# Kernel optimization log

Hardware: AMD Instinct MI355X
Metric: run time of the kernel (lower is better)

## Reference

```python
import jax, jax.numpy as jnp
import numpy as np
import math

B, P, N = 4, 8, 512
D_MODEL, H, D_K = 128, 4, 32
T_ALL = 4
WHICH_IDX = np.array([0, 1, 3])  # which_transition_matrices = [T,T,F,T]
T = 3
EPS = 1e-5


def setup_inputs() -> dict:
    key = jax.random.key(0)
    ks = jax.random.split(key, 12)
    inputs = jax.random.normal(ks[0], (B, P, N, D_MODEL), jnp.float32)
    c_inputs = jax.random.normal(ks[1], (B, P, N, D_MODEL), jnp.float32)
    vals = jax.random.uniform(ks[2], (T_ALL, N, N), jnp.float32)
    keep = (jax.random.uniform(ks[3], (T_ALL, N, N)) < 0.05).astype(jnp.float32)
    eye = jnp.eye(N, dtype=jnp.float32)
    transition_matrices = vals * keep * (1.0 - eye) + eye
    s = 1.0 / math.sqrt(D_MODEL)
    Wq = jax.random.normal(ks[4], (T, D_MODEL, D_MODEL), jnp.float32) * s
    Wk = jax.random.normal(ks[5], (T, D_MODEL, D_MODEL), jnp.float32) * s
    Wv = jax.random.normal(ks[6], (T, D_MODEL, D_MODEL), jnp.float32) * s
    Wo = jax.random.normal(ks[7], (D_MODEL, T * D_MODEL), jnp.float32) * (1.0 / math.sqrt(T * D_MODEL))
    ln_gamma = jnp.ones((D_MODEL,), jnp.float32)
    ln_beta = jnp.zeros((D_MODEL,), jnp.float32)
    return dict(inputs=inputs, c_inputs=c_inputs, transition_matrices=transition_matrices,
                Wq=Wq, Wk=Wk, Wv=Wv, Wo=Wo, ln_gamma=ln_gamma, ln_beta=ln_beta)


def reference(inputs, c_inputs, transition_matrices, Wq, Wk, Wv, Wo, ln_gamma, ln_beta):
    tm = transition_matrices[jnp.asarray(WHICH_IDX)]  # [T, N, N]
    # per-transition-matrix projections (torch Linear: x @ W.T), then split heads
    def proj(W):
        y = jnp.einsum('bpnd,tod->tbpno', inputs, W)
        return y.reshape(T, B, P, N, H, D_K)
    Q, K, V = proj(Wq), proj(Wk), proj(Wv)
    scores = jnp.einsum('tbpnhk,tbpmhk->tbphnm', Q, K) / math.sqrt(D_K)
    mask = jnp.where(tm != 0, 0.0, -jnp.inf)[:, None, None, None]  # [T,1,1,1,N,N]
    alpha = jax.nn.softmax(scores + mask, axis=-1)
    # post-softmax reweighting by transition matrix, then V matmul
    out = jnp.einsum('tbphnm,tbpmhk->tbpnhk', alpha * tm[:, None, None, None], V)
    out = out.reshape(T, B, P, N, D_MODEL)
    out = jnp.moveaxis(out, 0, -2).reshape(B, P, N, T * D_MODEL)  # concat over matrices
    out = jnp.einsum('bpnf,df->bpnd', out, Wo)  # final Linear (bias=False); dropout p=0
    res = out + inputs
    mu = res.mean(-1, keepdims=True)
    var = ((res - mu) ** 2).mean(-1, keepdims=True)
    return (res - mu) / jnp.sqrt(var + EPS) * ln_gamma + ln_beta
```

## Files before the change

### kernel.cpp

```cpp
#include <hip/hip_runtime.h>


typedef __attribute__((ext_vector_type(8))) short  short8;
typedef __attribute__((ext_vector_type(4))) float  floatx4;

#define WS_BIG   50331648ull
#define WS_XL    54919168ull
#define QSCALE   0.25503486f

__device__ __forceinline__ float b2f(unsigned short u) {
    union { unsigned int i; float f; } v; v.i = ((unsigned int)u) << 16; return v.f;
}
__device__ __forceinline__ unsigned short f2b(float f) {
    union { float f; unsigned int i; } v; v.f = f;
    unsigned int x = v.i;
    return (unsigned short)((x + 0x7fffu + ((x >> 16) & 1u)) >> 16);
}
__device__ __forceinline__ short8 cvt8(const float* p) {
    floatx4 a = *(const floatx4*)p;
    floatx4 b = *(const floatx4*)(p + 4);
    short8 r;
    r[0] = (short)f2b(a[0]); r[1] = (short)f2b(a[1]);
    r[2] = (short)f2b(a[2]); r[3] = (short)f2b(a[3]);
    r[4] = (short)f2b(b[0]); r[5] = (short)f2b(b[1]);
    r[6] = (short)f2b(b[2]); r[7] = (short)f2b(b[3]);
    return r;
}

__global__ __launch_bounds__(256) void k_prep(
    const float* __restrict__ X,  const float* __restrict__ Wq,
    const float* __restrict__ Wk, const float* __restrict__ Wv,
    const float* __restrict__ Wo,
    unsigned short* __restrict__ Xb, unsigned short* __restrict__ Wb,
    unsigned short* __restrict__ Wob)
{
    size_t i = ((size_t)blockIdx.x * 256 + threadIdx.x) * 8;
    const float* src; unsigned short* dst; size_t off;
    if      (i < 2097152) { src = X;  dst = Xb;          off = i; }
    else if (i < 2146304) { src = Wq; dst = Wb;          off = i - 2097152; }
    else if (i < 2195456) { src = Wk; dst = Wb + 49152;  off = i - 2146304; }
    else if (i < 2244608) { src = Wv; dst = Wb + 98304;  off = i - 2195456; }
    else                  { src = Wo; dst = Wob;         off = i - 2244608; }
    *(short8*)&dst[off] = cvt8(&src[off]);
}

__global__ __launch_bounds__(256) void k_qkv_pre(
    const unsigned short* __restrict__ Xb,
    const unsigned short* __restrict__ Wb,
    unsigned short* __restrict__ q_ws,
    unsigned short* __restrict__ k_ws,
    unsigned short* __restrict__ v_ws)
{
    int bp = blockIdx.x, mt = blockIdx.y, tz = blockIdx.z;
    __shared__ unsigned short Xs[128 * 128];
    int tid = threadIdx.x;
    int lane = tid & 63, wv = tid >> 6;
    int l15 = lane & 15, quad = lane >> 4;

    const unsigned short* Xbase = Xb + ((size_t)bp * 512 + mt * 128) * 128;
    for (int i = 0; i < 8; ++i) {
        int e = (i * 256 + tid) * 8;
        *(short8*)&Xs[e] = *(const short8*)&Xbase[e];
    }
    __syncthreads();

    unsigned short* Osel[3] = { q_ws, k_ws, v_ws };
    for (int qkv = 0; qkv < 3; ++qkv) {
        const unsigned short* Wt = Wb + qkv * 49152 + tz * 16384;
        unsigned short* Ob = Osel[qkv] + (size_t)tz * 2097152
                           + ((size_t)bp * 512 + mt * 128) * 128;
        float sc = (qkv == 0) ? QSCALE : 1.0f;
        for (int ct = 0; ct < 8; ++ct) {
            short8 bfr[4];
            for (int kk = 0; kk < 4; ++kk)
                bfr[kk] = *(const short8*)&Wt[(size_t)(ct * 16 + l15) * 128 + kk * 32 + quad * 8];
            floatx4 acc0 = {0.f, 0.f, 0.f, 0.f};
            floatx4 acc1 = {0.f, 0.f, 0.f, 0.f};
            int rt0 = wv * 2, rt1 = wv * 2 + 1;
            for (int kk = 0; kk < 4; ++kk) {
                short8 a0 = *(const short8*)&Xs[(rt0 * 16 + l15) * 128 + kk * 32 + quad * 8];
                short8 a1 = *(const short8*)&Xs[(rt1 * 16 + l15) * 128 + kk * 32 + quad * 8];
                acc0 = __builtin_amdgcn_mfma_f32_16x16x32_bf16(a0, bfr[kk], acc0, 0, 0, 0);
                acc1 = __builtin_amdgcn_mfma_f32_16x16x32_bf16(a1, bfr[kk], acc1, 0, 0, 0);
            }
            int col = ct * 16 + l15;
            for (int i = 0; i < 4; ++i) {
                Ob[(size_t)(rt0 * 16 + quad * 4 + i) * 128 + col] = f2b(acc0[i] * sc);
                Ob[(size_t)(rt1 * 16 + quad * 4 + i) * 128 + col] = f2b(acc1[i] * sc);
            }
        }
    }
}

__global__ __launch_bounds__(256) void k_qkv_cvt(
    const float* __restrict__ X,
    const float* __restrict__ Wq, const float* __restrict__ Wk,
    const float* __restrict__ Wv,
    unsigned short* __restrict__ q_ws, unsigned short* __restrict__ k_ws,
    unsigned short* __restrict__ v_ws,
    int wstride, int ostride)
{
    int bp = blockIdx.x, mt = blockIdx.y, tz = blockIdx.z;
    __shared__ unsigned short Xs[128 * 128];
    int tid = threadIdx.x;
    int lane = tid & 63, wv = tid >> 6;
    int l15 = lane & 15, quad = lane >> 4;

    const float* Xbase = X + ((size_t)bp * 512 + mt * 128) * 128;
    for (int i = 0; i < 8; ++i) {
        int e = (i * 256 + tid) * 8;
        *(short8*)&Xs[e] = cvt8(&Xbase[e]);
    }
    __syncthreads();

    size_t woff = (size_t)tz * wstride;
    size_t ooff = (size_t)tz * ostride;
    const float* Wsel[3] = { Wq + woff, Wk + woff, Wv + woff };
    unsigned short* Osel[3] = { q_ws + ooff, k_ws + ooff, v_ws + ooff };

    for (int qkv = 0; qkv < 3; ++qkv) {
        const float* Wb = Wsel[qkv];
        unsigned short* Ob = Osel[qkv] + ((size_t)bp * 512 + mt * 128) * 128;
        float sc = (qkv == 0) ? QSCALE : 1.0f;
        for (int ct = 0; ct < 8; ++ct) {
            short8 bfr[4];
            for (int kk = 0; kk < 4; ++kk)
                bfr[kk] = cvt8(&Wb[(size_t)(ct * 16 + l15) * 128 + kk * 32 + quad * 8]);
            floatx4 acc0 = {0.f, 0.f, 0.f, 0.f};
            floatx4 acc1 = {0.f, 0.f, 0.f, 0.f};
            int rt0 = wv * 2, rt1 = wv * 2 + 1;
            for (int kk = 0; kk < 4; ++kk) {
                short8 a0 = *(const short8*)&Xs[(rt0 * 16 + l15) * 128 + kk * 32 + quad * 8];
                short8 a1 = *(const short8*)&Xs[(rt1 * 16 + l15) * 128 + kk * 32 + quad * 8];
                acc0 = __builtin_amdgcn_mfma_f32_16x16x32_bf16(a0, bfr[kk], acc0, 0, 0, 0);
                acc1 = __builtin_amdgcn_mfma_f32_16x16x32_bf16(a1, bfr[kk], acc1, 0, 0, 0);
            }
            int col = ct * 16 + l15;
            for (int i = 0; i < 4; ++i) {
                Ob[(size_t)(rt0 * 16 + quad * 4 + i) * 128 + col] = f2b(acc0[i] * sc);
                Ob[(size_t)(rt1 * 16 + quad * 4 + i) * 128 + col] = f2b(acc1[i] * sc);
            }
        }
    }
}

__global__ __launch_bounds__(512) void k_attn(
    const unsigned short* __restrict__ q_ws,
    const unsigned short* __restrict__ k_ws,
    const unsigned short* __restrict__ v_ws,
    const float* __restrict__ tm,
    unsigned short* __restrict__ att_ws,
    int qkv_stride, int toff0)
{
    int nc = blockIdx.x;
    int bp = blockIdx.y;
    int z  = blockIdx.z;
    int t = z >> 2, h = z & 3;
    size_t qoff = (size_t)t * (size_t)qkv_stride;
    const float* tmt = tm + (size_t)(t + (t >> 1)) * 262144;
    int toff = toff0 + t * 128;

    __shared__ unsigned short Vt[32][516];
    __shared__ unsigned short Ps[8][16][72];

    int tid = threadIdx.x, lane = tid & 63, wv = tid >> 6;
    int l15 = lane & 15, quad = lane >> 4;

    {
        const unsigned short* vp = v_ws + qoff + ((size_t)bp * 512 + tid) * 128 + h * 32;
        short8 a = *(const short8*)vp;
        short8 b = *(const short8*)(vp + 8);
        short8 c = *(const short8*)(vp + 16);
        short8 d = *(const short8*)(vp + 24);
        #pragma unroll
        for (int j = 0; j < 8; ++j) {
            Vt[j][tid]      = (unsigned short)a[j];
            Vt[8 + j][tid]  = (unsigned short)b[j];
            Vt[16 + j][tid] = (unsigned short)c[j];
            Vt[24 + j][tid] = (unsigned short)d[j];
        }
    }
    int n0 = nc * 128 + wv * 16;
    short8 qf = *(const short8*)&q_ws[qoff +
        ((size_t)bp * 512 + n0 + l15) * 128 + h * 32 + quad * 8];
    __syncthreads();

    const unsigned short* Kb = k_ws + qoff + (size_t)bp * 512 * 128 + h * 32;
    floatx4 O0 = {0.f, 0.f, 0.f, 0.f};
    floatx4 O1 = {0.f, 0.f, 0.f, 0.f};
    float za[4] = {0.f, 0.f, 0.f, 0.f};
    const floatx4 zero4 = {0.f, 0.f, 0.f, 0.f};

    for (int c = 0; c < 8; ++c) {
        int mb = c * 64;
        short8 kf0 = *(const short8*)&Kb[(size_t)(mb +  0 + l15) * 128 + quad * 8];
        short8 kf1 = *(const short8*)&Kb[(size_t)(mb + 16 + l15) * 128 + quad * 8];
        short8 kf2 = *(const short8*)&Kb[(size_t)(mb + 32 + l15) * 128 + quad * 8];
        short8 kf3 = *(const short8*)&Kb[(size_t)(mb + 48 + l15) * 128 + quad * 8];
        floatx4 S[4];
        S[0] = __builtin_amdgcn_mfma_f32_16x16x32_bf16(qf, kf0, zero4, 0, 0, 0);
        S[1] = __builtin_amdgcn_mfma_f32_16x16x32_bf16(qf, kf1, zero4, 0, 0, 0);
        S[2] = __builtin_amdgcn_mfma_f32_16x16x32_bf16(qf, kf2, zero4, 0, 0, 0);
        S[3] = __builtin_amdgcn_mfma_f32_16x16x32_bf16(qf, kf3, zero4, 0, 0, 0);

        #pragma unroll
        for (int ti = 0; ti < 4; ++ti) {
            int m = mb + ti * 16 + l15;
            #pragma unroll
            for (int i = 0; i < 4; ++i) {
                float tmv = tmt[(size_t)(n0 + quad * 4 + i) * 512 + m];
                float e = __builtin_amdgcn_exp2f(S[ti][i]);
                bool on = (tmv != 0.0f);
                za[i] += on ? e : 0.0f;
                float w = on ? e * tmv : 0.0f;
                Ps[wv][quad * 4 + i][ti * 16 + l15] = f2b(w);
            }
        }
        #pragma unroll
        for (int kc = 0; kc < 2; ++kc) {
            short8 pa  = *(const short8*)&Ps[wv][l15][kc * 32 + quad * 8];
            short8 vb0 = *(const short8*)&Vt[l15][mb + kc * 32 + quad * 8];
            short8 vb1 = *(const short8*)&Vt[16 + l15][mb + kc * 32 + quad * 8];
            O0 = __builtin_amdgcn_mfma_f32_16x16x32_bf16(pa, vb0, O0, 0, 0, 0);
            O1 = __builtin_amdgcn_mfma_f32_16x16x32_bf16(pa, vb1, O1, 0, 0, 0);
        }
    }

    #pragma unroll
    for (int d = 1; d < 16; d <<= 1) {
        #pragma unroll
        for (int i = 0; i < 4; ++i) za[i] += __shfl_xor(za[i], d, 64);
    }
    #pragma unroll
    for (int i = 0; i < 4; ++i) {
        float rz = 1.0f / za[i];
        size_t row = (size_t)bp * 512 + n0 + quad * 4 + i;
        att_ws[row * 384 + toff + h * 32 + l15]      = f2b(O0[i] * rz);
        att_ws[row * 384 + toff + h * 32 + 16 + l15] = f2b(O1[i] * rz);
    }
}

__global__ __launch_bounds__(256) void k_oproj_pre(
    const unsigned short* __restrict__ att_ws,
    const unsigned short* __restrict__ Wob,
    const float* __restrict__ X,
    const float* __restrict__ gamma,
    const float* __restrict__ beta,
    float* __restrict__ out)
{
    int bp = blockIdx.x;
    int mt = blockIdx.y;
    __shared__ unsigned short As[64 * 128];
    __shared__ unsigned short Ws[128 * 128];
    int tid = threadIdx.x, lane = tid & 63, wv = tid >> 6;
    int l15 = lane & 15, quad = lane >> 4;

    floatx4 acc[8];
    for (int ct = 0; ct < 8; ++ct) acc[ct] = (floatx4){0.f, 0.f, 0.f, 0.f};
    size_t rowbase = (size_t)bp * 512 + mt * 64;

    for (int kc = 0; kc < 3; ++kc) {
        __syncthreads();
        for (int i = 0; i < 4; ++i) {
            int flat = i * 256 + tid;
            int row = flat >> 4, colg = (flat & 15) * 8;
            *(short8*)&As[row * 128 + colg] =
                *(const short8*)&att_ws[(rowbase + row) * 384 + kc * 128 + colg];
        }
        for (int i = 0; i < 8; ++i) {
            int flat = i * 256 + tid;
            int row = flat >> 4, colg = (flat & 15) * 8;
            *(short8*)&Ws[row * 128 + colg] =
                *(const short8*)&Wob[(size_t)row * 384 + kc * 128 + colg];
        }
        __syncthreads();
        for (int ct = 0; ct < 8; ++ct) {
            for (int kk = 0; kk < 4; ++kk) {
                short8 a = *(const short8*)&As[(wv * 16 + l15) * 128 + kk * 32 + quad * 8];
                short8 b = *(const short8*)&Ws[(ct * 16 + l15) * 128 + kk * 32 + quad * 8];
                acc[ct] = __builtin_amdgcn_mfma_f32_16x16x32_bf16(a, b, acc[ct], 0, 0, 0);
            }
        }
    }

    for (int i = 0; i < 4; ++i) {
        int lrow = wv * 16 + quad * 4 + i;
        size_t grow = rowbase + lrow;
        float vals[8];
        float s = 0.f, sq = 0.f;
        for (int ct = 0; ct < 8; ++ct) {
            int col = ct * 16 + l15;
            float v = acc[ct][i] + X[grow * 128 + col];
            vals[ct] = v;
            s += v; sq += v * v;
        }
        for (int d = 1; d < 16; d <<= 1) {
            s  += __shfl_xor(s, d, 64);
            sq += __shfl_xor(sq, d, 64);
        }
        float mu = s * (1.0f / 128.0f);
        float var = sq * (1.0f / 128.0f) - mu * mu;
        float rs = rsqrtf(var + 1e-5f);
        for (int ct = 0; ct < 8; ++ct) {
            int col = ct * 16 + l15;
            out[grow * 128 + col] = (vals[ct] - mu) * rs * gamma[col] + beta[col];
        }
    }
}

__global__ __launch_bounds__(256) void k_oproj_cvt(
    const unsigned short* __restrict__ att_ws,
    const float* __restrict__ Wo,
    const float* __restrict__ X,
    const float* __restrict__ gamma,
    const float* __restrict__ beta,
    float* __restrict__ out)
{
    int bp = blockIdx.x;
    int mt = blockIdx.y;
    __shared__ unsigned short As[64 * 128];
    __shared__ unsigned short Ws[128 * 128];
    int tid = threadIdx.x, lane = tid & 63, wv = tid >> 6;
    int l15 = lane & 15, quad = lane >> 4;

    floatx4 acc[8];
    for (int ct = 0; ct < 8; ++ct) acc[ct] = (floatx4){0.f, 0.f, 0.f, 0.f};
    size_t rowbase = (size_t)bp * 512 + mt * 64;

    for (int kc = 0; kc < 3; ++kc) {
        __syncthreads();
        for (int i = 0; i < 4; ++i) {
            int flat = i * 256 + tid;
            int row = flat >> 4, colg = (flat & 15) * 8;
            *(short8*)&As[row * 128 + colg] =
                *(const short8*)&att_ws[(rowbase + row) * 384 + kc * 128 + colg];
        }
        for (int i = 0; i < 8; ++i) {
            int flat = i * 256 + tid;
            int row = flat >> 4, colg = (flat & 15) * 8;
            *(short8*)&Ws[row * 128 + colg] = cvt8(&Wo[(size_t)row * 384 + kc * 128 + colg]);
        }
        __syncthreads();
        for (int ct = 0; ct < 8; ++ct) {
            for (int kk = 0; kk < 4; ++kk) {
                short8 a = *(const short8*)&As[(wv * 16 + l15) * 128 + kk * 32 + quad * 8];
                short8 b = *(const short8*)&Ws[(ct * 16 + l15) * 128 + kk * 32 + quad * 8];
                acc[ct] = __builtin_amdgcn_mfma_f32_16x16x32_bf16(a, b, acc[ct], 0, 0, 0);
            }
        }
    }

    for (int i = 0; i < 4; ++i) {
        int lrow = wv * 16 + quad * 4 + i;
        size_t grow = rowbase + lrow;
        float vals[8];
        float s = 0.f, sq = 0.f;
        for (int ct = 0; ct < 8; ++ct) {
            int col = ct * 16 + l15;
            float v = acc[ct][i] + X[grow * 128 + col];
            vals[ct] = v;
            s += v; sq += v * v;
        }
        for (int d = 1; d < 16; d <<= 1) {
            s  += __shfl_xor(s, d, 64);
            sq += __shfl_xor(sq, d, 64);
        }
        float mu = s * (1.0f / 128.0f);
        float var = sq * (1.0f / 128.0f) - mu * mu;
        float rs = rsqrtf(var + 1e-5f);
        for (int ct = 0; ct < 8; ++ct) {
            int col = ct * 16 + l15;
            out[grow * 128 + col] = (vals[ct] - mu) * rs * gamma[col] + beta[col];
        }
    }
}

extern "C" void kernel_launch(void* const* d_in, const int* in_sizes, int n_in,
                              void* d_out, int out_size, void* d_ws, size_t ws_size,
                              hipStream_t stream) {
    const float* X     = (const float*)d_in[0];
    const float* TM    = (const float*)d_in[2];
    const float* Wq    = (const float*)d_in[3];
    const float* Wk    = (const float*)d_in[4];
    const float* Wv    = (const float*)d_in[5];
    const float* Wo    = (const float*)d_in[6];
    const float* gamma = (const float*)d_in[7];
    const float* beta  = (const float*)d_in[8];
    float* out = (float*)d_out;

    char* ws = (char*)d_ws;
    const size_t QKV1 = 2097152;
    const size_t QKV1B = QKV1 * 2;

    if (ws_size >= WS_XL) {
        unsigned short* q3  = (unsigned short*)(ws);
        unsigned short* k3  = (unsigned short*)(ws + 3 * QKV1B);
        unsigned short* v3  = (unsigned short*)(ws + 6 * QKV1B);
        unsigned short* att = (unsigned short*)(ws + 9 * QKV1B);
        unsigned short* Xb  = (unsigned short*)(ws + 50331648ull);
        unsigned short* Wb  = (unsigned short*)(ws + 54525952ull);
        unsigned short* Wob = (unsigned short*)(ws + 54820864ull);
        k_prep<<<dim3(1120), 256, 0, stream>>>(X, Wq, Wk, Wv, Wo, Xb, Wb, Wob);
        k_qkv_pre<<<dim3(32, 4, 3), 256, 0, stream>>>(Xb, Wb, q3, k3, v3);
        k_attn<<<dim3(4, 32, 12), 512, 0, stream>>>(q3, k3, v3, TM, att, (int)QKV1, 0);
        k_oproj_pre<<<dim3(32, 8), 256, 0, stream>>>(att, Wob, X, gamma, beta, out);
    } else if (ws_size >= WS_BIG) {
        unsigned short* q3  = (unsigned short*)(ws);
        unsigned short* k3  = (unsigned short*)(ws + 3 * QKV1B);
        unsigned short* v3  = (unsigned short*)(ws + 6 * QKV1B);
        unsigned short* att = (unsigned short*)(ws + 9 * QKV1B);
        k_qkv_cvt<<<dim3(32, 4, 3), 256, 0, stream>>>(
            X, Wq, Wk, Wv, q3, k3, v3, 16384, (int)QKV1);
        k_attn<<<dim3(4, 32, 12), 512, 0, stream>>>(q3, k3, v3, TM, att, (int)QKV1, 0);
        k_oproj_cvt<<<dim3(32, 8), 256, 0, stream>>>(att, Wo, X, gamma, beta, out);
    } else {
        unsigned short* q_ws   = (unsigned short*)(ws);
        unsigned short* k_ws   = (unsigned short*)(ws + QKV1B);
        unsigned short* v_ws   = (unsigned short*)(ws + 2 * QKV1B);
        unsigned short* att_ws = (unsigned short*)(ws + 3 * QKV1B);
        const int tsel[3] = {0, 1, 3};
        for (int t = 0; t < 3; ++t) {
            k_qkv_cvt<<<dim3(32, 4, 1), 256, 0, stream>>>(
                X, Wq + (size_t)t * 16384, Wk + (size_t)t * 16384, Wv + (size_t)t * 16384,
                q_ws, k_ws, v_ws, 0, 0);
            k_attn<<<dim3(4, 32, 4), 512, 0, stream>>>(
                q_ws, k_ws, v_ws, TM + (size_t)tsel[t] * 262144, att_ws, 0, t * 128);
        }
        k_oproj_cvt<<<dim3(32, 8), 256, 0, stream>>>(att_ws, Wo, X, gamma, beta, out);
    }
}
```

Baseline: 191.0 us.

## Pre-transpose transition matrices to bf16 and widen QKV/oproj grids

The prep kernel no longer converts X to bf16. Instead it transposes the three selected transition matrices into bf16 so the attention kernel can read a column-contiguous 4-element vector per lane instead of strided fp32 values. The QKV kernel now splits q/k/v across the grid z dimension (9 slices) and converts X inline. The output projection uses 32-row tiles with a cross-wave LayerNorm reduction through shared memory, which doubles its block count. The costs are redundant X conversion across the 9 z-slices and bf16 rounding of the transition weights.

```diff
diff --git a/kernel.cpp b/kernel.cpp
--- a/kernel.cpp
+++ b/kernel.cpp
@@ -3,9 +3,10 @@
 
 typedef __attribute__((ext_vector_type(8))) short  short8;
 typedef __attribute__((ext_vector_type(4))) float  floatx4;
+typedef __attribute__((ext_vector_type(4))) unsigned short u16x4;
 
 #define WS_BIG   50331648ull
-#define WS_XL    54919168ull
+#define WS_XL    52297728ull
 #define QSCALE   0.25503486f
 
 __device__ __forceinline__ float b2f(unsigned short u) {
@@ -15,6 +16,9 @@
     union { float f; unsigned int i; } v; v.f = f;
     unsigned int x = v.i;
     return (unsigned short)((x + 0x7fffu + ((x >> 16) & 1u)) >> 16);
+}
+__device__ __forceinline__ unsigned int fbits(float f) {
+    union { float f; unsigned int i; } v; v.f = f; return v.i;
 }
 __device__ __forceinline__ short8 cvt8(const float* p) {
     floatx4 a = *(const floatx4*)p;
@@ -28,28 +32,106 @@
 }
 
 __global__ __launch_bounds__(256) void k_prep(
-    const float* __restrict__ X,  const float* __restrict__ Wq,
-    const float* __restrict__ Wk, const float* __restrict__ Wv,
-    const float* __restrict__ Wo,
-    unsigned short* __restrict__ Xb, unsigned short* __restrict__ Wb,
-    unsigned short* __restrict__ Wob)
-{
-    size_t i = ((size_t)blockIdx.x * 256 + threadIdx.x) * 8;
-    const float* src; unsigned short* dst; size_t off;
-    if      (i < 2097152) { src = X;  dst = Xb;          off = i; }
-    else if (i < 2146304) { src = Wq; dst = Wb;          off = i - 2097152; }
-    else if (i < 2195456) { src = Wk; dst = Wb + 49152;  off = i - 2146304; }
-    else if (i < 2244608) { src = Wv; dst = Wb + 98304;  off = i - 2195456; }
-    else                  { src = Wo; dst = Wob;         off = i - 2244608; }
-    *(short8*)&dst[off] = cvt8(&src[off]);
-}
-
-__global__ __launch_bounds__(256) void k_qkv_pre(
-    const unsigned short* __restrict__ Xb,
+    const float* __restrict__ Wq, const float* __restrict__ Wk,
+    const float* __restrict__ Wv, const float* __restrict__ Wo,
+    const float* __restrict__ TM,
+    unsigned short* __restrict__ Wb,
+    unsigned short* __restrict__ Wob,
+    unsigned short* __restrict__ tmT)
+{
+    int bid = blockIdx.x, tid = threadIdx.x;
+    if (bid < 96) {
+        size_t i = (size_t)bid * 2048 + tid * 8;
+        const float* src; unsigned short* dst; size_t off;
+        if      (i <  49152) { src = Wq; dst = Wb;          off = i; }
+        else if (i <  98304) { src = Wk; dst = Wb + 49152;  off = i - 49152; }
+        else if (i < 147456) { src = Wv; dst = Wb + 98304;  off = i - 98304; }
+        else                 { src = Wo; dst = Wob;         off = i - 147456; }
+        *(short8*)&dst[off] = cvt8(&src[off]);
+        return;
+    }
+    __shared__ float Tl[64][65];
+    int r = bid - 96;
+    int t = r >> 6, tile = r & 63;
+    int ntile = tile >> 3, mtile = tile & 7;
+    const float* tmsrc = TM + (size_t)(t + (t >> 1)) * 262144;
+    {
+        int row = tid >> 2, cseg = (tid & 3) * 16;
+        const float* p = &tmsrc[(size_t)(ntile * 64 + row) * 512 + mtile * 64 + cseg];
+        #pragma unroll
+        for (int j = 0; j < 4; ++j)
+            *(floatx4*)&Tl[row][cseg + j * 4] = *(const floatx4*)&p[j * 4];
+    }
+    __syncthreads();
+    {
+        int m = tid >> 2, nseg = (tid & 3) * 16;
+        unsigned short* q = &tmT[(size_t)t * 262144 +
+                                 (size_t)(mtile * 64 + m) * 512 + ntile * 64 + nseg];
+        short8 o0, o1;
+        #pragma unroll
+        for (int j = 0; j < 8; ++j) {
+            o0[j] = (short)f2b(Tl[nseg + j][m]);
+            o1[j] = (short)f2b(Tl[nseg + 8 + j][m]);
+        }
+        *(short8*)&q[0] = o0;
+        *(short8*)&q[8] = o1;
+    }
+}
+
+__global__ __launch_bounds__(256) void k_qkv2(
+    const float* __restrict__ X,
     const unsigned short* __restrict__ Wb,
     unsigned short* __restrict__ q_ws,
     unsigned short* __restrict__ k_ws,
     unsigned short* __restrict__ v_ws)
+{
+    int bp = blockIdx.x, mt = blockIdx.y, z = blockIdx.z;
+    int t = z / 3, qkv = z - t * 3;
+    __shared__ unsigned short Xs[128 * 128];
+    int tid = threadIdx.x;
+    int lane = tid & 63, wv = tid >> 6;
+    int l15 = lane & 15, quad = lane >> 4;
+
+    const float* Xbase = X + ((size_t)bp * 512 + mt * 128) * 128;
+    for (int i = 0; i < 8; ++i) {
+        int e = (i * 256 + tid) * 8;
+        *(short8*)&Xs[e] = cvt8(&Xbase[e]);
+    }
+    __syncthreads();
+
+    const unsigned short* Wt = Wb + qkv * 49152 + t * 16384;
+    unsigned short* Ob = (qkv == 0 ? q_ws : qkv == 1 ? k_ws : v_ws)
+                       + (size_t)t * 2097152 + ((size_t)bp * 512 + mt * 128) * 128;
+    float sc = (qkv == 0) ? QSCALE : 1.0f;
+
+    for (int ct = 0; ct < 8; ++ct) {
+        short8 bfr[4];
+        for (int kk = 0; kk < 4; ++kk)
+            bfr[kk] = *(const short8*)&Wt[(size_t)(ct * 16 + l15) * 128 + kk * 32 + quad * 8];
+        floatx4 acc0 = {0.f, 0.f, 0.f, 0.f};
+        floatx4 acc1 = {0.f, 0.f, 0.f, 0.f};
+        int rt0 = wv * 2, rt1 = wv * 2 + 1;
+        for (int kk = 0; kk < 4; ++kk) {
+            short8 a0 = *(const short8*)&Xs[(rt0 * 16 + l15) * 128 + kk * 32 + quad * 8];
+            short8 a1 = *(const short8*)&Xs[(rt1 * 16 + l15) * 128 + kk * 32 + quad * 8];
+            acc0 = __builtin_amdgcn_mfma_f32_16x16x32_bf16(a0, bfr[kk], acc0, 0, 0, 0);
+            acc1 = __builtin_amdgcn_mfma_f32_16x16x32_bf16(a1, bfr[kk], acc1, 0, 0, 0);
+        }
+        int col = ct * 16 + l15;
+        for (int i = 0; i < 4; ++i) {
+            Ob[(size_t)(rt0 * 16 + quad * 4 + i) * 128 + col] = f2b(acc0[i] * sc);
+            Ob[(size_t)(rt1 * 16 + quad * 4 + i) * 128 + col] = f2b(acc1[i] * sc);
+        }
+    }
+}
+
+__global__ __launch_bounds__(256) void k_qkv_cvt(
+    const float* __restrict__ X,
+    const float* __restrict__ Wq, const float* __restrict__ Wk,
+    const float* __restrict__ Wv,
+    unsigned short* __restrict__ q_ws, unsigned short* __restrict__ k_ws,
+    unsigned short* __restrict__ v_ws,
+    int wstride, int ostride)
 {
     int bp = blockIdx.x, mt = blockIdx.y, tz = blockIdx.z;
     __shared__ unsigned short Xs[128 * 128];
@@ -57,23 +139,26 @@
     int lane = tid & 63, wv = tid >> 6;
     int l15 = lane & 15, quad = lane >> 4;
 
-    const unsigned short* Xbase = Xb + ((size_t)bp * 512 + mt * 128) * 128;
+    const float* Xbase = X + ((size_t)bp * 512 + mt * 128) * 128;
     for (int i = 0; i < 8; ++i) {
         int e = (i * 256 + tid) * 8;
-        *(short8*)&Xs[e] = *(const short8*)&Xbase[e];
+        *(short8*)&Xs[e] = cvt8(&Xbase[e]);
     }
     __syncthreads();
 
-    unsigned short* Osel[3] = { q_ws, k_ws, v_ws };
+    size_t woff = (size_t)tz * wstride;
+    size_t ooff = (size_t)tz * ostride;
+    const float* Wsel[3] = { Wq + woff, Wk + woff, Wv + woff };
+    unsigned short* Osel[3] = { q_ws + ooff, k_ws + ooff, v_ws + ooff };
+
     for (int qkv = 0; qkv < 3; ++qkv) {
-        const unsigned short* Wt = Wb + qkv * 49152 + tz * 16384;
-        unsigned short* Ob = Osel[qkv] + (size_t)tz * 2097152
-                           + ((size_t)bp * 512 + mt * 128) * 128;
+        const float* Wt = Wsel[qkv];
+        unsigned short* Ob = Osel[qkv] + ((size_t)bp * 512 + mt * 128) * 128;
         float sc = (qkv == 0) ? QSCALE : 1.0f;
         for (int ct = 0; ct < 8; ++ct) {
             short8 bfr[4];
             for (int kk = 0; kk < 4; ++kk)
-                bfr[kk] = *(const short8*)&Wt[(size_t)(ct * 16 + l15) * 128 + kk * 32 + quad * 8];
+                bfr[kk] = cvt8(&Wt[(size_t)(ct * 16 + l15) * 128 + kk * 32 + quad * 8]);
             floatx4 acc0 = {0.f, 0.f, 0.f, 0.f};
             floatx4 acc1 = {0.f, 0.f, 0.f, 0.f};
             int rt0 = wv * 2, rt1 = wv * 2 + 1;
@@ -92,59 +177,105 @@
     }
 }
 
-__global__ __launch_bounds__(256) void k_qkv_cvt(
-    const float* __restrict__ X,
-    const float* __restrict__ Wq, const float* __restrict__ Wk,
-    const float* __restrict__ Wv,
-    unsigned short* __restrict__ q_ws, unsigned short* __restrict__ k_ws,
-    unsigned short* __restrict__ v_ws,
-    int wstride, int ostride)
-{
-    int bp = blockIdx.x, mt = blockIdx.y, tz = blockIdx.z;
-    __shared__ unsigned short Xs[128 * 128];
-    int tid = threadIdx.x;
-    int lane = tid & 63, wv = tid >> 6;
+__global__ __launch_bounds__(512) void k_attn_t(
+    const unsigned short* __restrict__ q_ws,
+    const unsigned short* __restrict__ k_ws,
+    const unsigned short* __restrict__ v_ws,
+    const unsigned short* __restrict__ tmT,
+    unsigned short* __restrict__ att_ws)
+{
+    int nc = blockIdx.x;
+    int bp = blockIdx.y;
+    int z  = blockIdx.z;
+    int t = z >> 2, h = z & 3;
+    size_t qoff = (size_t)t * 2097152;
+    const unsigned short* tmt = tmT + (size_t)t * 262144;
+
+    __shared__ unsigned short Vt[32][516];
+    __shared__ unsigned short Ps[8][16][72];
+
+    int tid = threadIdx.x, lane = tid & 63, wv = tid >> 6;
     int l15 = lane & 15, quad = lane >> 4;
 
-    const float* Xbase = X + ((size_t)bp * 512 + mt * 128) * 128;
-    for (int i = 0; i < 8; ++i) {
-        int e = (i * 256 + tid) * 8;
-        *(short8*)&Xs[e] = cvt8(&Xbase[e]);
-    }
+    {
+        const unsigned short* vp = v_ws + qoff + ((size_t)bp * 512 + tid) * 128 + h * 32;
+        short8 a = *(const short8*)vp;
+        short8 b = *(const short8*)(vp + 8);
+        short8 c = *(const short8*)(vp + 16);
+        short8 d = *(const short8*)(vp + 24);
+        #pragma unroll
+        for (int j = 0; j < 8; ++j) {
+            Vt[j][tid]      = (unsigned short)a[j];
+            Vt[8 + j][tid]  = (unsigned short)b[j];
+            Vt[16 + j][tid] = (unsigned short)c[j];
+            Vt[24 + j][tid] = (unsigned short)d[j];
+        }
+    }
+    int n0 = nc * 128 + wv * 16;
+    short8 qf = *(const short8*)&q_ws[qoff +
+        ((size_t)bp * 512 + n0 + l15) * 128 + h * 32 + quad * 8];
     __syncthreads();
 
-    size_t woff = (size_t)tz * wstride;
-    size_t ooff = (size_t)tz * ostride;
-    const float* Wsel[3] = { Wq + woff, Wk + woff, Wv + woff };
-    unsigned short* Osel[3] = { q_ws + ooff, k_ws + ooff, v_ws + ooff };
-
-    for (int qkv = 0; qkv < 3; ++qkv) {
-        const float* Wb = Wsel[qkv];
-        unsigned short* Ob = Osel[qkv] + ((size_t)bp * 512 + mt * 128) * 128;
-        float sc = (qkv == 0) ? QSCALE : 1.0f;
-        for (int ct = 0; ct < 8; ++ct) {
-            short8 bfr[4];
-            for (int kk = 0; kk < 4; ++kk)
-                bfr[kk] = cvt8(&Wb[(size_t)(ct * 16 + l15) * 128 + kk * 32 + quad * 8]);
-            floatx4 acc0 = {0.f, 0.f, 0.f, 0.f};
-            floatx4 acc1 = {0.f, 0.f, 0.f, 0.f};
-            int rt0 = wv * 2, rt1 = wv * 2 + 1;
-            for (int kk = 0; kk < 4; ++kk) {
-                short8 a0 = *(const short8*)&Xs[(rt0 * 16 + l15) * 128 + kk * 32 + quad * 8];
-                short8 a1 = *(const short8*)&Xs[(rt1 * 16 + l15) * 128 + kk * 32 + quad * 8];
-                acc0 = __builtin_amdgcn_mfma_f32_16x16x32_bf16(a0, bfr[kk], acc0, 0, 0, 0);
-                acc1 = __builtin_amdgcn_mfma_f32_16x16x32_bf16(a1, bfr[kk], acc1, 0, 0, 0);
+    const unsigned short* Kb = k_ws + qoff + (size_t)bp * 512 * 128 + h * 32;
+    floatx4 O0 = {0.f, 0.f, 0.f, 0.f};
+    floatx4 O1 = {0.f, 0.f, 0.f, 0.f};
+    float za[4] = {0.f, 0.f, 0.f, 0.f};
+    const floatx4 zero4 = {0.f, 0.f, 0.f, 0.f};
+
+    for (int c = 0; c < 8; ++c) {
+        int mb = c * 64;
+        short8 kf0 = *(const short8*)&Kb[(size_t)(mb +  0 + l15) * 128 + quad * 8];
+        short8 kf1 = *(const short8*)&Kb[(size_t)(mb + 16 + l15) * 128 + quad * 8];
+        short8 kf2 = *(const short8*)&Kb[(size_t)(mb + 32 + l15) * 128 + quad * 8];
+        short8 kf3 = *(const short8*)&Kb[(size_t)(mb + 48 + l15) * 128 + quad * 8];
+        u16x4 t4[4];
+        #pragma unroll
+        for (int ti = 0; ti < 4; ++ti)
+            t4[ti] = *(const u16x4*)&tmt[(size_t)(mb + ti * 16 + l15) * 512 + n0 + quad * 4];
+        floatx4 S[4];
+        S[0] = __builtin_amdgcn_mfma_f32_16x16x32_bf16(qf, kf0, zero4, 0, 0, 0);
+        S[1] = __builtin_amdgcn_mfma_f32_16x16x32_bf16(qf, kf1, zero4, 0, 0, 0);
+        S[2] = __builtin_amdgcn_mfma_f32_16x16x32_bf16(qf, kf2, zero4, 0, 0, 0);
+        S[3] = __builtin_amdgcn_mfma_f32_16x16x32_bf16(qf, kf3, zero4, 0, 0, 0);
+
+        #pragma unroll
+        for (int ti = 0; ti < 4; ++ti) {
+            #pragma unroll
+            for (int i = 0; i < 4; ++i) {
+                unsigned short tv = t4[ti][i];
+                float e = __builtin_amdgcn_exp2f(S[ti][i]);
+                bool on = (tv != 0);
+                za[i] += on ? e : 0.0f;
+                float w = on ? e * b2f(tv) : 0.0f;
+                Ps[wv][quad * 4 + i][ti * 16 + l15] =
+                    (unsigned short)((fbits(w) + 0x8000u) >> 16);
             }
-            int col = ct * 16 + l15;
-            for (int i = 0; i < 4; ++i) {
-                Ob[(size_t)(rt0 * 16 + quad * 4 + i) * 128 + col] = f2b(acc0[i] * sc);
-                Ob[(size_t)(rt1 * 16 + quad * 4 + i) * 128 + col] = f2b(acc1[i] * sc);
-            }
-        }
-    }
-}
-
-__global__ __launch_bounds__(512) void k_attn(
+        }
+        #pragma unroll
+        for (int kc = 0; kc < 2; ++kc) {
+            short8 pa  = *(const short8*)&Ps[wv][l15][kc * 32 + quad * 8];
+            short8 vb0 = *(const short8*)&Vt[l15][mb + kc * 32 + quad * 8];
+            short8 vb1 = *(const short8*)&Vt[16 + l15][mb + kc * 32 + quad * 8];
+            O0 = __builtin_amdgcn_mfma_f32_16x16x32_bf16(pa, vb0, O0, 0, 0, 0);
+            O1 = __builtin_amdgcn_mfma_f32_16x16x32_bf16(pa, vb1, O1, 0, 0, 0);
+        }
+    }
+
+    #pragma unroll
+    for (int d = 1; d < 16; d <<= 1) {
+        #pragma unroll
+        for (int i = 0; i < 4; ++i) za[i] += __shfl_xor(za[i], d, 64);
+    }
+    #pragma unroll
+    for (int i = 0; i < 4; ++i) {
+        float rz = 1.0f / za[i];
+        size_t row = (size_t)bp * 512 + n0 + quad * 4 + i;
+        att_ws[row * 384 + t * 128 + h * 32 + l15]      = f2b(O0[i] * rz);
+        att_ws[row * 384 + t * 128 + h * 32 + 16 + l15] = f2b(O1[i] * rz);
+    }
+}
+
+__global__ __launch_bounds__(512) void k_attn_f32(
     const unsigned short* __restrict__ q_ws,
     const unsigned short* __restrict__ k_ws,
     const unsigned short* __restrict__ v_ws,
@@ -240,7 +371,7 @@
     }
 }
 
-__global__ __launch_bounds__(256) void k_oproj_pre(
+__global__ __launch_bounds__(256) void k_oproj2(
     const unsigned short* __restrict__ att_ws,
     const unsigned short* __restrict__ Wob,
     const float* __restrict__ X,
@@ -250,18 +381,20 @@
 {
     int bp = blockIdx.x;
     int mt = blockIdx.y;
-    __shared__ unsigned short As[64 * 128];
+    __shared__ unsigned short As[32 * 128];
     __shared__ unsigned short Ws[128 * 128];
+    __shared__ float psum[2][2][16][2];
     int tid = threadIdx.x, lane = tid & 63, wv = tid >> 6;
     int l15 = lane & 15, quad = lane >> 4;
-
-    floatx4 acc[8];
-    for (int ct = 0; ct < 8; ++ct) acc[ct] = (floatx4){0.f, 0.f, 0.f, 0.f};
-    size_t rowbase = (size_t)bp * 512 + mt * 64;
+    int rt = wv >> 1, ch = wv & 1;
+
+    floatx4 acc[4];
+    for (int c4 = 0; c4 < 4; ++c4) acc[c4] = (floatx4){0.f, 0.f, 0.f, 0.f};
+    size_t rowbase = (size_t)bp * 512 + mt * 32;
 
     for (int kc = 0; kc < 3; ++kc) {
         __syncthreads();
-        for (int i = 0; i < 4; ++i) {
+        for (int i = 0; i < 2; ++i) {
             int flat = i * 256 + tid;
             int row = flat >> 4, colg = (flat & 15) * 8;
             *(short8*)&As[row * 128 + colg] =
@@ -274,36 +407,47 @@
                 *(const short8*)&Wob[(size_t)row * 384 + kc * 128 + colg];
         }
         __syncthreads();
-        for (int ct = 0; ct < 8; ++ct) {
+        for (int c4 = 0; c4 < 4; ++c4) {
+            int ct = ch * 4 + c4;
             for (int kk = 0; kk < 4; ++kk) {
-                short8 a = *(const short8*)&As[(wv * 16 + l15) * 128 + kk * 32 + quad * 8];
+                short8 a = *(const short8*)&As[(rt * 16 + l15) * 128 + kk * 32 + quad * 8];
                 short8 b = *(const short8*)&Ws[(ct * 16 + l15) * 128 + kk * 32 + quad * 8];
-                acc[ct] = __builtin_amdgcn_mfma_f32_16x16x32_bf16(a, b, acc[ct], 0, 0, 0);
+                acc[c4] = __builtin_amdgcn_mfma_f32_16x16x32_bf16(a, b, acc[c4], 0, 0, 0);
             }
         }
     }
 
+    float vals[4][4], ssum[4], qsum[4];
     for (int i = 0; i < 4; ++i) {
-        int lrow = wv * 16 + quad * 4 + i;
-        size_t grow = rowbase + lrow;
-        float vals[8];
+        size_t grow = rowbase + rt * 16 + quad * 4 + i;
         float s = 0.f, sq = 0.f;
-        for (int ct = 0; ct < 8; ++ct) {
-            int col = ct * 16 + l15;
-            float v = acc[ct][i] + X[grow * 128 + col];
-            vals[ct] = v;
+        for (int c4 = 0; c4 < 4; ++c4) {
+            int col = (ch * 4 + c4) * 16 + l15;
+            float v = acc[c4][i] + X[grow * 128 + col];
+            vals[i][c4] = v;
             s += v; sq += v * v;
         }
         for (int d = 1; d < 16; d <<= 1) {
             s  += __shfl_xor(s, d, 64);
             sq += __shfl_xor(sq, d, 64);
         }
+        ssum[i] = s; qsum[i] = sq;
+        if (l15 == 0) {
+            psum[ch][rt][quad * 4 + i][0] = s;
+            psum[ch][rt][quad * 4 + i][1] = sq;
+        }
+    }
+    __syncthreads();
+    for (int i = 0; i < 4; ++i) {
+        size_t grow = rowbase + rt * 16 + quad * 4 + i;
+        float s  = ssum[i] + psum[ch ^ 1][rt][quad * 4 + i][0];
+        float sq = qsum[i] + psum[ch ^ 1][rt][quad * 4 + i][1];
         float mu = s * (1.0f / 128.0f);
         float var = sq * (1.0f / 128.0f) - mu * mu;
         float rs = rsqrtf(var + 1e-5f);
-        for (int ct = 0; ct < 8; ++ct) {
-            int col = ct * 16 + l15;
-            out[grow * 128 + col] = (vals[ct] - mu) * rs * gamma[col] + beta[col];
+        for (int c4 = 0; c4 < 4; ++c4) {
+            int col = (ch * 4 + c4) * 16 + l15;
+            out[grow * 128 + col] = (vals[i][c4] - mu) * rs * gamma[col] + beta[col];
         }
     }
 }
@@ -393,17 +537,17 @@
     const size_t QKV1B = QKV1 * 2;
 
     if (ws_size >= WS_XL) {
-        unsigned short* q3  = (unsigned short*)(ws);
-        unsigned short* k3  = (unsigned short*)(ws + 3 * QKV1B);
-        unsigned short* v3  = (unsigned short*)(ws + 6 * QKV1B);
-        unsigned short* att = (unsigned short*)(ws + 9 * QKV1B);
-        unsigned short* Xb  = (unsigned short*)(ws + 50331648ull);
-        unsigned short* Wb  = (unsigned short*)(ws + 54525952ull);
-        unsigned short* Wob = (unsigned short*)(ws + 54820864ull);
-        k_prep<<<dim3(1120), 256, 0, stream>>>(X, Wq, Wk, Wv, Wo, Xb, Wb, Wob);
-        k_qkv_pre<<<dim3(32, 4, 3), 256, 0, stream>>>(Xb, Wb, q3, k3, v3);
-        k_attn<<<dim3(4, 32, 12), 512, 0, stream>>>(q3, k3, v3, TM, att, (int)QKV1, 0);
-        k_oproj_pre<<<dim3(32, 8), 256, 0, stream>>>(att, Wob, X, gamma, beta, out);
+        unsigned short* q3   = (unsigned short*)(ws);
+        unsigned short* k3   = (unsigned short*)(ws + 3 * QKV1B);
+        unsigned short* v3   = (unsigned short*)(ws + 6 * QKV1B);
+        unsigned short* att  = (unsigned short*)(ws + 9 * QKV1B);
+        unsigned short* Wb   = (unsigned short*)(ws + 50331648ull);
+        unsigned short* Wob  = (unsigned short*)(ws + 50626560ull);
+        unsigned short* tmTb = (unsigned short*)(ws + 50724864ull);
+        k_prep<<<dim3(288), 256, 0, stream>>>(Wq, Wk, Wv, Wo, TM, Wb, Wob, tmTb);
+        k_qkv2<<<dim3(32, 4, 9), 256, 0, stream>>>(X, Wb, q3, k3, v3);
+        k_attn_t<<<dim3(4, 32, 12), 512, 0, stream>>>(q3, k3, v3, tmTb, att);
+        k_oproj2<<<dim3(32, 16), 256, 0, stream>>>(att, Wob, X, gamma, beta, out);
     } else if (ws_size >= WS_BIG) {
         unsigned short* q3  = (unsigned short*)(ws);
         unsigned short* k3  = (unsigned short*)(ws + 3 * QKV1B);
@@ -411,7 +555,7 @@
         unsigned short* att = (unsigned short*)(ws + 9 * QKV1B);
         k_qkv_cvt<<<dim3(32, 4, 3), 256, 0, stream>>>(
             X, Wq, Wk, Wv, q3, k3, v3, 16384, (int)QKV1);
-        k_attn<<<dim3(4, 32, 12), 512, 0, stream>>>(q3, k3, v3, TM, att, (int)QKV1, 0);
+        k_attn_f32<<<dim3(4, 32, 12), 512, 0, stream>>>(q3, k3, v3, TM, att, (int)QKV1, 0);
         k_oproj_cvt<<<dim3(32, 8), 256, 0, stream>>>(att, Wo, X, gamma, beta, out);
     } else {
         unsigned short* q_ws   = (unsigned short*)(ws);
@@ -423,7 +567,7 @@
             k_qkv_cvt<<<dim3(32, 4, 1), 256, 0, stream>>>(
                 X, Wq + (size_t)t * 16384, Wk + (size_t)t * 16384, Wv + (size_t)t * 16384,
                 q_ws, k_ws, v_ws, 0, 0);
-            k_attn<<<dim3(4, 32, 4), 512, 0, stream>>>(
+            k_attn_f32<<<dim3(4, 32, 4), 512, 0, stream>>>(
                 q_ws, k_ws, v_ws, TM + (size_t)tsel[t] * 262144, att_ws, 0, t * 128);
         }
         k_oproj_cvt<<<dim3(32, 8), 256, 0, stream>>>(att_ws, Wo, X, gamma, beta, out);
```

Measured after the change: 218.6 us. 14.5% more time.
